# Optimization experiments

Hardware: AMD Instinct MI355X
Metric: run time of the kernel (lower is better)

The kernel has to match this reference:

```python
import jax, jax.numpy as jnp
import numpy as np

N_NODES = 100000


def _gcn_layer(x, W, b, row, col, ew, n):
    # PyG GCNConv: x' = D^{-1/2} (A + I) D^{-1/2} (x W) + b
    xw = x @ W  # [N, out]
    deg = jax.ops.segment_sum(ew, col, num_segments=n)  # weighted in-degree incl. self loops
    dinv = jnp.where(deg > 0, jax.lax.rsqrt(deg), 0.0)
    norm = dinv[row] * ew * dinv[col]  # [E]
    msg = xw[row] * norm[:, None]  # [E, out] gather + scale
    out = jax.ops.segment_sum(msg, col, num_segments=n) + b
    return out


def setup_inputs() -> dict:
    key = jax.random.key(0)
    k = jax.random.split(key, 6)
    E = 1600000
    h = 64
    x = jax.random.normal(k[0], (N_NODES, 4), dtype=jnp.float32)
    edge_index = jax.random.randint(k[1], (2, E), 0, N_NODES, dtype=jnp.int64)
    edge_weight = jax.random.uniform(k[2], (E,), dtype=jnp.float32)
    W1 = jax.random.normal(k[3], (4, h), dtype=jnp.float32) * (1.0 / np.sqrt(4))
    b1 = jnp.zeros((h,), dtype=jnp.float32)
    W2 = jax.random.normal(k[4], (h, h), dtype=jnp.float32) * (1.0 / np.sqrt(h))
    b2 = jnp.zeros((h,), dtype=jnp.float32)
    return {"x": x, "edge_index": edge_index, "edge_weight": edge_weight,
            "W1": W1, "b1": b1, "W2": W2, "b2": b2}


def reference(x, edge_index, edge_weight, W1, b1, W2, b2):
    n = x.shape[0]
    # add self loops with weight 1 (GCNConv default add_self_loops=True)
    loop = jnp.arange(n, dtype=edge_index.dtype)
    row = jnp.concatenate([edge_index[0], loop])
    col = jnp.concatenate([edge_index[1], loop])
    ew = jnp.concatenate([edge_weight, jnp.ones((n,), dtype=edge_weight.dtype)])
    h = jax.nn.relu(_gcn_layer(x, W1, b1, row, col, ew, n))
    out = jax.nn.relu(_gcn_layer(h, W2, b2, row, col, ew, n))
    return out
```

## Files before the change

kernel.cpp:

```cpp
#include <hip/hip_runtime.h>

#define H 64
#define BKT_SHIFT 7
#define BKT_NODES 128
#define NB 782
#define CAP 2432
#define SC_K 16
#define SC_T 256
#define SC_TILE (SC_K * SC_T)

typedef __attribute__((ext_vector_type(8))) short short8v;
typedef __attribute__((ext_vector_type(4))) float float4v;

__device__ __forceinline__ float bf2f(unsigned short u) {
    return __uint_as_float(((unsigned)u) << 16);
}
__device__ __forceinline__ unsigned short f2bf(float f) {
    unsigned u = __float_as_uint(f);
    unsigned r = ((u >> 16) & 1u) + 0x7FFFu;
    return (unsigned short)((u + r) >> 16);
}
__device__ __forceinline__ float bflo(unsigned d) { return __uint_as_float(d << 16); }
__device__ __forceinline__ float bfhi(unsigned d) { return __uint_as_float(d & 0xFFFF0000u); }


__global__ void k_prep(const float* __restrict__ W2, unsigned* __restrict__ cursor,
                       unsigned short* __restrict__ W2Tb) {
    int g = blockIdx.x * 256 + threadIdx.x;
    if (g < NB) cursor[g] = (unsigned)g * CAP;
    if (g < H * H) {
        int c = g >> 6, k = g & 63;
        W2Tb[g] = f2bf(W2[k * H + c]);
    }
}


__global__ __launch_bounds__(SC_T) void k_bscatter(
        const int* __restrict__ row, const int* __restrict__ col,
        const float* __restrict__ ew, unsigned* __restrict__ cursor,
        uint2* __restrict__ sorted, int E) {
    __shared__ unsigned hist[NB];
    __shared__ unsigned gbase[NB];
    int t = threadIdx.x;
    for (int b = t; b < NB; b += SC_T) hist[b] = 0;
    __syncthreads();
    int tile = blockIdx.x * SC_TILE;
    unsigned st[SC_K];
#pragma unroll
    for (int k = 0; k < SC_K; ++k) {
        int e = tile + k * SC_T + t;
        unsigned enc = 0xFFFFFFFFu;
        if (e < E) {
            unsigned c = (unsigned)col[e];
            unsigned b = c >> BKT_SHIFT;
            unsigned nl = c & (BKT_NODES - 1);
            unsigned r = atomicAdd(&hist[b], 1u);
            enc = (b << 20) | (nl << 13) | r;
        }
        st[k] = enc;
    }
    __syncthreads();
    for (int b = t; b < NB; b += SC_T) {
        unsigned h = hist[b];
        if (h) gbase[b] = atomicAdd(&cursor[b], h);
    }
    __syncthreads();
#pragma unroll
    for (int k = 0; k < SC_K; ++k) {
        int e = tile + k * SC_T + t;
        if (e >= E) continue;
        unsigned enc = st[k];
        unsigned b = enc >> 20, nl = (enc >> 13) & 127u, r = enc & 8191u;
        unsigned pk = ((unsigned)row[e] << 7) | nl;
        sorted[gbase[b] + r] = make_uint2(pk, __float_as_uint(ew[e]));
    }
}


__global__ __launch_bounds__(256) void k_bsort(const uint2* __restrict__ sorted,
                                               const unsigned* __restrict__ cursor,
                                               const float* __restrict__ x,
                                               uint2* __restrict__ sorted2,
                                               unsigned* __restrict__ startA,
                                               unsigned* __restrict__ cntA,
                                               float* __restrict__ dinv,
                                               unsigned short* __restrict__ xqb, int n) {
    __shared__ unsigned hist[BKT_NODES];
    __shared__ unsigned base_[BKT_NODES];
    __shared__ float deg[BKT_NODES];
    __shared__ unsigned wsum;
    int b = blockIdx.x, t = threadIdx.x;
    if (t < BKT_NODES) { hist[t] = 0; deg[t] = 1.0f; }
    __syncthreads();
    unsigned s = (unsigned)b * CAP, e = cursor[b];
    uint2 st[10];
#pragma unroll
    for (int k = 0; k < 10; ++k) {
        unsigned j = s + (unsigned)t + ((unsigned)k << 8);
        if (j < e) {
            uint2 u = sorted[j];
            st[k] = u;
            unsigned nl = u.x & 127u;
            atomicAdd(&hist[nl], 1u);
            atomicAdd(&deg[nl], __uint_as_float(u.y));
        }
    }
    __syncthreads();
    if (t < BKT_NODES) {
        unsigned v = hist[t];
        unsigned sc = v;
#pragma unroll
        for (int d = 1; d < 64; d <<= 1) {
            unsigned u = __shfl_up(sc, d);
            if ((t & 63) >= d) sc += u;
        }
        if (t == 63) wsum = sc;
        base_[t] = sc - v;
        int node = b * BKT_NODES + t;
        if (node < n) {
            cntA[node] = v;
            float di = rsqrtf(deg[t]);
            dinv[node] = di;
            float4 xv = ((const float4*)x)[node];
            ushort4 o;
            o.x = f2bf(xv.x * di); o.y = f2bf(xv.y * di);
            o.z = f2bf(xv.z * di); o.w = f2bf(xv.w * di);
            ((ushort4*)xqb)[node] = o;
        }
        hist[t] = 0;
    }
    __syncthreads();
    if (t >= 64 && t < BKT_NODES) base_[t] += wsum;
    __syncthreads();
    if (t < BKT_NODES) {
        int node = b * BKT_NODES + t;
        if (node < n) startA[node] = s + base_[t];
    }
    __syncthreads();
#pragma unroll
    for (int k = 0; k < 10; ++k) {
        unsigned j = s + (unsigned)t + ((unsigned)k << 8);
        if (j < e) {
            uint2 u = st[k];
            unsigned nl = u.x & 127u;
            unsigned pos = atomicAdd(&hist[nl], 1u);
            sorted2[s + base_[nl] + pos] = make_uint2(u.x & 0xFFFFFF80u, u.y);
        }
    }
}


__global__ __launch_bounds__(256) void k_agg1(const uint2* __restrict__ sorted2,
                                              const unsigned* __restrict__ startA,
                                              const unsigned* __restrict__ cntA,
                                              const float* __restrict__ dinv,
                                              const unsigned short* __restrict__ xqb,
                                              const float* __restrict__ W1,
                                              const float* __restrict__ b1,
                                              unsigned short* __restrict__ hb, int n) {
    __shared__ float w1s[4 * H];
    __shared__ float b1s[H];
    int t = threadIdx.x;
    if (t < 4 * H) w1s[t] = W1[t];
    if (t < H) b1s[t] = b1[t];
    __syncthreads();
    int wv = (int)(__builtin_amdgcn_readfirstlane(threadIdx.x) >> 6);
    int wid = blockIdx.x * 4 + wv;
    if (wid >= n) return;
    int lane = t & 63;
    int eg = lane >> 1, f2 = lane & 1;
    unsigned s = startA[wid];
    unsigned cnt = cntA[wid];
    float aLo = 0.0f, aHi = 0.0f;
    const char* xq = (const char*)xqb + (f2 << 2);
    for (unsigned b = 0; b < cnt; b += 32) {
        unsigned i = b + (unsigned)eg;
        bool v = i < cnt;
        uint2 p = sorted2[s + (v ? i : 0u)];
        float w = v ? __uint_as_float(p.y) : 0.0f;
        unsigned d = *(const unsigned*)(xq + (p.x >> 4));
        aLo = fmaf(bflo(d), w, aLo);
        aHi = fmaf(bfhi(d), w, aHi);
    }
    aLo += __shfl_xor(aLo, 2);  aHi += __shfl_xor(aHi, 2);
    aLo += __shfl_xor(aLo, 4);  aHi += __shfl_xor(aHi, 4);
    aLo += __shfl_xor(aLo, 8);  aHi += __shfl_xor(aHi, 8);
    aLo += __shfl_xor(aLo, 16); aHi += __shfl_xor(aHi, 16);
    aLo += __shfl_xor(aLo, 32); aHi += __shfl_xor(aHi, 32);
    float a0 = __shfl(aLo, 0), a1 = __shfl(aHi, 0);
    float a2 = __shfl(aLo, 1), a3 = __shfl(aHi, 1);
    uint2 sq = *(const uint2*)(xqb + ((size_t)wid << 2));
    a0 += bflo(sq.x); a1 += bfhi(sq.x);
    a2 += bflo(sq.y); a3 += bfhi(sq.y);
    float hv = a0 * w1s[lane] + a1 * w1s[H + lane] + a2 * w1s[2 * H + lane]
             + a3 * w1s[3 * H + lane];
    hv = dinv[wid] * hv + b1s[lane];
    hb[((size_t)wid << 6) + lane] = f2bf(fmaxf(hv, 0.0f));
}


__global__ __launch_bounds__(256) void k_l2mfma(const unsigned short* __restrict__ hb,
                                                const unsigned short* __restrict__ W2Tb,
                                                const float* __restrict__ dinv,
                                                unsigned short* __restrict__ xs2b, int n) {
    __shared__ unsigned short ht[128 * H];
    __shared__ unsigned short wt[H * H];
    int tid = threadIdx.x;
    int base = blockIdx.x * 128;
    for (int idx = tid; idx < 1024; idx += 256) {
        int r = idx >> 3, c = idx & 7;
        uint4 v = *(const uint4*)(hb + (((size_t)(base + r)) << 6) + (c << 3));
        *(uint4*)(ht + (r << 6) + ((c ^ (r & 7)) << 3)) = v;
    }
    for (int idx = tid; idx < 512; idx += 256) {
        int r = idx >> 3, c = idx & 7;
        uint4 v = *(const uint4*)(W2Tb + (r << 6) + (c << 3));
        *(uint4*)(wt + (r << 6) + ((c ^ (r & 7)) << 3)) = v;
    }
    __syncthreads();
    int lane = tid & 63;
    int wv = tid >> 6;
    int R = wv * 32;
    int lr = lane & 15, lq = lane >> 4;
    short8v a[2][2], b[4][2];
#pragma unroll
    for (int m = 0; m < 2; ++m)
#pragma unroll
        for (int kk = 0; kk < 2; ++kk) {
            int row = R + m * 16 + lr;
            int cl = kk * 4 + lq;
            a[m][kk] = *(const short8v*)(ht + (row << 6) + ((cl ^ (row & 7)) << 3));
        }
#pragma unroll
    for (int nt = 0; nt < 4; ++nt)
#pragma unroll
        for (int kk = 0; kk < 2; ++kk) {
            int row = nt * 16 + lr;
            int cl = kk * 4 + lq;
            b[nt][kk] = *(const short8v*)(wt + (row << 6) + ((cl ^ (row & 7)) << 3));
        }
    float4v acc[2][4] = {};
#pragma unroll
    for (int m = 0; m < 2; ++m)
#pragma unroll
        for (int nt = 0; nt < 4; ++nt)
#pragma unroll
            for (int kk = 0; kk < 2; ++kk)
                acc[m][nt] = __builtin_amdgcn_mfma_f32_16x16x32_bf16(a[m][kk], b[nt][kk],
                                                                     acc[m][nt], 0, 0, 0);
#pragma unroll
    for (int m = 0; m < 2; ++m)
#pragma unroll
        for (int i = 0; i < 4; ++i) {
            int node = base + R + m * 16 + lq * 4 + i;
            if (node < n) {
                float di = dinv[node];
#pragma unroll
                for (int nt = 0; nt < 4; ++nt)
                    xs2b[((size_t)node << 6) + nt * 16 + lr] = f2bf(acc[m][nt][i] * di);
            }
        }
}


__global__ __launch_bounds__(256) void k_agg2(const uint2* __restrict__ sorted2,
                                              const unsigned* __restrict__ startA,
                                              const unsigned* __restrict__ cntA,
                                              const float* __restrict__ dinv,
                                              const unsigned short* __restrict__ xsb,
                                              const float* __restrict__ bias,
                                              float* __restrict__ outf, int n) {
    int wv = (int)(__builtin_amdgcn_readfirstlane(threadIdx.x) >> 6);
    int wid = blockIdx.x * 4 + wv;
    if (wid >= n) return;
    int lane = threadIdx.x & 63;
    int eg = lane >> 3;
    int c8 = lane & 7;
    unsigned s = startA[wid];
    unsigned cnt = cntA[wid];
    float di = dinv[wid];
    const char* xb = (const char*)xsb + (c8 << 4);
    float a0=0.f,a1=0.f,a2=0.f,a3=0.f,a4=0.f,a5=0.f,a6=0.f,a7=0.f;
    for (unsigned b = 0; b < cnt; b += 16) {
        unsigned iA = b + (unsigned)eg;
        bool vA = iA < cnt;
        uint2 pA = sorted2[s + (vA ? iA : 0u)];
        float wA = vA ? __uint_as_float(pA.y) : 0.0f;
        uint4 dA = *(const uint4*)(xb + pA.x);
        unsigned iB = iA + 8u;
        bool vB = iB < cnt;
        uint2 pB = sorted2[s + (vB ? iB : 0u)];
        float wB = vB ? __uint_as_float(pB.y) : 0.0f;
        uint4 dB = *(const uint4*)(xb + pB.x);
        a0 = fmaf(bflo(dA.x), wA, a0); a1 = fmaf(bfhi(dA.x), wA, a1);
        a2 = fmaf(bflo(dA.y), wA, a2); a3 = fmaf(bfhi(dA.y), wA, a3);
        a4 = fmaf(bflo(dA.z), wA, a4); a5 = fmaf(bfhi(dA.z), wA, a5);
        a6 = fmaf(bflo(dA.w), wA, a6); a7 = fmaf(bfhi(dA.w), wA, a7);
        a0 = fmaf(bflo(dB.x), wB, a0); a1 = fmaf(bfhi(dB.x), wB, a1);
        a2 = fmaf(bflo(dB.y), wB, a2); a3 = fmaf(bfhi(dB.y), wB, a3);
        a4 = fmaf(bflo(dB.z), wB, a4); a5 = fmaf(bfhi(dB.z), wB, a5);
        a6 = fmaf(bflo(dB.w), wB, a6); a7 = fmaf(bfhi(dB.w), wB, a7);
    }
    a0 += __shfl_xor(a0, 8); a0 += __shfl_xor(a0, 16); a0 += __shfl_xor(a0, 32);
    a1 += __shfl_xor(a1, 8); a1 += __shfl_xor(a1, 16); a1 += __shfl_xor(a1, 32);
    a2 += __shfl_xor(a2, 8); a2 += __shfl_xor(a2, 16); a2 += __shfl_xor(a2, 32);
    a3 += __shfl_xor(a3, 8); a3 += __shfl_xor(a3, 16); a3 += __shfl_xor(a3, 32);
    a4 += __shfl_xor(a4, 8); a4 += __shfl_xor(a4, 16); a4 += __shfl_xor(a4, 32);
    a5 += __shfl_xor(a5, 8); a5 += __shfl_xor(a5, 16); a5 += __shfl_xor(a5, 32);
    a6 += __shfl_xor(a6, 8); a6 += __shfl_xor(a6, 16); a6 += __shfl_xor(a6, 32);
    a7 += __shfl_xor(a7, 8); a7 += __shfl_xor(a7, 16); a7 += __shfl_xor(a7, 32);
    uint4 sv = *(const uint4*)((const char*)xsb + (((size_t)(unsigned)wid) << 7) + (c8 << 4));
    a0 += bflo(sv.x); a1 += bfhi(sv.x);
    a2 += bflo(sv.y); a3 += bfhi(sv.y);
    a4 += bflo(sv.z); a5 += bfhi(sv.z);
    a6 += bflo(sv.w); a7 += bfhi(sv.w);
    const float* bp = bias + (c8 << 3);
    float r0 = fmaxf(di * a0 + bp[0], 0.0f);
    float r1 = fmaxf(di * a1 + bp[1], 0.0f);
    float r2 = fmaxf(di * a2 + bp[2], 0.0f);
    float r3 = fmaxf(di * a3 + bp[3], 0.0f);
    float r4 = fmaxf(di * a4 + bp[4], 0.0f);
    float r5 = fmaxf(di * a5 + bp[5], 0.0f);
    float r6 = fmaxf(di * a6 + bp[6], 0.0f);
    float r7 = fmaxf(di * a7 + bp[7], 0.0f);
    if (eg == 0) {
        float4 o = {r0, r1, r2, r3};
        *(float4*)(outf + (((size_t)wid) << 6) + (c8 << 3)) = o;
    } else if (eg == 1) {
        float4 o = {r4, r5, r6, r7};
        *(float4*)(outf + (((size_t)wid) << 6) + (c8 << 3) + 4) = o;
    }
}


extern "C" void kernel_launch(void* const* d_in, const int* in_sizes, int n_in,
                              void* d_out, int out_size, void* d_ws, size_t ws_size,
                              hipStream_t stream) {
    const float* x  = (const float*)d_in[0];
    const int*   ei = (const int*)d_in[1];
    const float* ew = (const float*)d_in[2];
    const float* W1 = (const float*)d_in[3];
    const float* b1 = (const float*)d_in[4];
    const float* W2 = (const float*)d_in[5];
    const float* b2 = (const float*)d_in[6];
    float* out = (float*)d_out;

    const int n = in_sizes[0] / 4;
    const int E = in_sizes[2];
    const int* row = ei;
    const int* col = ei + E;

    char* p = (char*)d_ws;
    unsigned* cursor = (unsigned*)p;            p += 1024 * 4;
    unsigned short* W2Tb = (unsigned short*)p;  p += (size_t)H * H * 2;
    float* dinv      = (float*)p;               p += (size_t)n * 4;
    unsigned* startA = (unsigned*)p;            p += (size_t)n * 4;
    unsigned* cntA   = (unsigned*)p;            p += (size_t)n * 4;
    unsigned short* xqb = (unsigned short*)p;   p += (size_t)n * 4 * 2;
    unsigned short* hb  = (unsigned short*)p;   p += ((size_t)n + 128) * H * 2;
    unsigned short* xs2b = (unsigned short*)p;  p += (size_t)n * H * 2;
    uint2* sorted    = (uint2*)p;               p += ((size_t)NB * CAP + 64) * 8;
    uint2* sorted2   = (uint2*)p;

    k_prep<<<16, 256, 0, stream>>>(W2, cursor, W2Tb);

    k_bscatter<<<(E + SC_TILE - 1) / SC_TILE, SC_T, 0, stream>>>(row, col, ew, cursor, sorted, E);

    k_bsort<<<NB, 256, 0, stream>>>(sorted, cursor, x, sorted2, startA, cntA, dinv, xqb, n);

    int aggBlocks = (n + 3) / 4;
    k_agg1<<<aggBlocks, 256, 0, stream>>>(sorted2, startA, cntA, dinv, xqb, W1, b1, hb, n);

    k_l2mfma<<<(n + 127) / 128, 256, 0, stream>>>(hb, W2Tb, dinv, xs2b, n);

    k_agg2<<<aggBlocks, 256, 0, stream>>>(sorted2, startA, cntA, dinv, xs2b, b2, out, n);
}
```

Baseline: 149.6 us.

## Aggregate layer-1 per thread, fuse W1 transform into MFMA kernel, narrow agg2 lanes

```diff
diff --git a/kernel.cpp b/kernel.cpp
--- a/kernel.cpp
+++ b/kernel.cpp
@@ -153,69 +153,90 @@
 __global__ __launch_bounds__(256) void k_agg1(const uint2* __restrict__ sorted2,
                                               const unsigned* __restrict__ startA,
                                               const unsigned* __restrict__ cntA,
-                                              const float* __restrict__ dinv,
                                               const unsigned short* __restrict__ xqb,
-                                              const float* __restrict__ W1,
-                                              const float* __restrict__ b1,
-                                              unsigned short* __restrict__ hb, int n) {
+                                              float4* __restrict__ agg4, int n) {
+    int node = blockIdx.x * 256 + threadIdx.x;
+    if (node >= n) return;
+    unsigned s = startA[node];
+    unsigned cnt = cntA[node];
+    const char* xq = (const char*)xqb;
+    uint2 sq = *(const uint2*)(xqb + ((size_t)node << 2));
+    float a0 = bflo(sq.x), a1 = bfhi(sq.x), a2 = bflo(sq.y), a3 = bfhi(sq.y);
+    unsigned j = 0;
+    for (; j + 4 <= cnt; j += 4) {
+        uint2 p0 = sorted2[s + j + 0];
+        uint2 p1 = sorted2[s + j + 1];
+        uint2 p2 = sorted2[s + j + 2];
+        uint2 p3 = sorted2[s + j + 3];
+        uint2 q0 = *(const uint2*)(xq + (p0.x >> 4));
+        uint2 q1 = *(const uint2*)(xq + (p1.x >> 4));
+        uint2 q2 = *(const uint2*)(xq + (p2.x >> 4));
+        uint2 q3 = *(const uint2*)(xq + (p3.x >> 4));
+        float w0 = __uint_as_float(p0.y), w1 = __uint_as_float(p1.y);
+        float w2 = __uint_as_float(p2.y), w3 = __uint_as_float(p3.y);
+        a0 = fmaf(bflo(q0.x), w0, a0); a1 = fmaf(bfhi(q0.x), w0, a1);
+        a2 = fmaf(bflo(q0.y), w0, a2); a3 = fmaf(bfhi(q0.y), w0, a3);
+        a0 = fmaf(bflo(q1.x), w1, a0); a1 = fmaf(bfhi(q1.x), w1, a1);
+        a2 = fmaf(bflo(q1.y), w1, a2); a3 = fmaf(bfhi(q1.y), w1, a3);
+        a0 = fmaf(bflo(q2.x), w2, a0); a1 = fmaf(bfhi(q2.x), w2, a1);
+        a2 = fmaf(bflo(q2.y), w2, a2); a3 = fmaf(bfhi(q2.y), w2, a3);
+        a0 = fmaf(bflo(q3.x), w3, a0); a1 = fmaf(bfhi(q3.x), w3, a1);
+        a2 = fmaf(bflo(q3.y), w3, a2); a3 = fmaf(bfhi(q3.y), w3, a3);
+    }
+    for (; j < cnt; ++j) {
+        uint2 p = sorted2[s + j];
+        uint2 q = *(const uint2*)(xq + (p.x >> 4));
+        float w = __uint_as_float(p.y);
+        a0 = fmaf(bflo(q.x), w, a0); a1 = fmaf(bfhi(q.x), w, a1);
+        a2 = fmaf(bflo(q.y), w, a2); a3 = fmaf(bfhi(q.y), w, a3);
+    }
+    agg4[node] = make_float4(a0, a1, a2, a3);
+}
+
+
+__global__ __launch_bounds__(256) void k_l2front(const float4* __restrict__ agg4,
+                                                 const float* __restrict__ W1,
+                                                 const float* __restrict__ b1,
+                                                 const unsigned short* __restrict__ W2Tb,
+                                                 const float* __restrict__ dinv,
+                                                 unsigned short* __restrict__ xs2b, int n) {
+    __shared__ unsigned short ht[128 * H];
+    __shared__ unsigned short wt[H * H];
     __shared__ float w1s[4 * H];
     __shared__ float b1s[H];
-    int t = threadIdx.x;
-    if (t < 4 * H) w1s[t] = W1[t];
-    if (t < H) b1s[t] = b1[t];
-    __syncthreads();
-    int wv = (int)(__builtin_amdgcn_readfirstlane(threadIdx.x) >> 6);
-    int wid = blockIdx.x * 4 + wv;
-    if (wid >= n) return;
-    int lane = t & 63;
-    int eg = lane >> 1, f2 = lane & 1;
-    unsigned s = startA[wid];
-    unsigned cnt = cntA[wid];
-    float aLo = 0.0f, aHi = 0.0f;
-    const char* xq = (const char*)xqb + (f2 << 2);
-    for (unsigned b = 0; b < cnt; b += 32) {
-        unsigned i = b + (unsigned)eg;
-        bool v = i < cnt;
-        uint2 p = sorted2[s + (v ? i : 0u)];
-        float w = v ? __uint_as_float(p.y) : 0.0f;
-        unsigned d = *(const unsigned*)(xq + (p.x >> 4));
-        aLo = fmaf(bflo(d), w, aLo);
-        aHi = fmaf(bfhi(d), w, aHi);
-    }
-    aLo += __shfl_xor(aLo, 2);  aHi += __shfl_xor(aHi, 2);
-    aLo += __shfl_xor(aLo, 4);  aHi += __shfl_xor(aHi, 4);
-    aLo += __shfl_xor(aLo, 8);  aHi += __shfl_xor(aHi, 8);
-    aLo += __shfl_xor(aLo, 16); aHi += __shfl_xor(aHi, 16);
-    aLo += __shfl_xor(aLo, 32); aHi += __shfl_xor(aHi, 32);
-    float a0 = __shfl(aLo, 0), a1 = __shfl(aHi, 0);
-    float a2 = __shfl(aLo, 1), a3 = __shfl(aHi, 1);
-    uint2 sq = *(const uint2*)(xqb + ((size_t)wid << 2));
-    a0 += bflo(sq.x); a1 += bfhi(sq.x);
-    a2 += bflo(sq.y); a3 += bfhi(sq.y);
-    float hv = a0 * w1s[lane] + a1 * w1s[H + lane] + a2 * w1s[2 * H + lane]
-             + a3 * w1s[3 * H + lane];
-    hv = dinv[wid] * hv + b1s[lane];
-    hb[((size_t)wid << 6) + lane] = f2bf(fmaxf(hv, 0.0f));
-}
-
-
-__global__ __launch_bounds__(256) void k_l2mfma(const unsigned short* __restrict__ hb,
-                                                const unsigned short* __restrict__ W2Tb,
-                                                const float* __restrict__ dinv,
-                                                unsigned short* __restrict__ xs2b, int n) {
-    __shared__ unsigned short ht[128 * H];
-    __shared__ unsigned short wt[H * H];
     int tid = threadIdx.x;
     int base = blockIdx.x * 128;
-    for (int idx = tid; idx < 1024; idx += 256) {
-        int r = idx >> 3, c = idx & 7;
-        uint4 v = *(const uint4*)(hb + (((size_t)(base + r)) << 6) + (c << 3));
-        *(uint4*)(ht + (r << 6) + ((c ^ (r & 7)) << 3)) = v;
-    }
+    w1s[tid] = W1[tid];
+    if (tid < H) b1s[tid] = b1[tid];
     for (int idx = tid; idx < 512; idx += 256) {
         int r = idx >> 3, c = idx & 7;
         uint4 v = *(const uint4*)(W2Tb + (r << 6) + (c << 3));
         *(uint4*)(wt + (r << 6) + ((c ^ (r & 7)) << 3)) = v;
+    }
+    __syncthreads();
+    {
+        int r = tid >> 1, ch = tid & 1;
+        int node = base + r;
+        float4 av = (node < n) ? agg4[node] : make_float4(0.f, 0.f, 0.f, 0.f);
+        float di = (node < n) ? dinv[node] : 0.0f;
+#pragma unroll
+        for (int cc = 0; cc < 4; ++cc) {
+            int cl = ch * 4 + cc;
+            uint4 ov;
+            unsigned* op = (unsigned*)&ov;
+#pragma unroll
+            for (int d = 0; d < 4; ++d) {
+                int col = (cl << 3) + (d << 1);
+                float h0 = av.x * w1s[col]     + av.y * w1s[H + col]
+                         + av.z * w1s[2*H+col] + av.w * w1s[3*H + col];
+                float h1 = av.x * w1s[col+1]     + av.y * w1s[H + col+1]
+                         + av.z * w1s[2*H+col+1] + av.w * w1s[3*H + col+1];
+                h0 = fmaxf(di * h0 + b1s[col], 0.0f);
+                h1 = fmaxf(di * h1 + b1s[col + 1], 0.0f);
+                op[d] = ((unsigned)f2bf(h1) << 16) | f2bf(h0);
+            }
+            *(uint4*)(ht + (r << 6) + ((cl ^ (r & 7)) << 3)) = ov;
+        }
     }
     __syncthreads();
     int lane = tid & 63;
@@ -274,61 +295,44 @@
     int wid = blockIdx.x * 4 + wv;
     if (wid >= n) return;
     int lane = threadIdx.x & 63;
-    int eg = lane >> 3;
-    int c8 = lane & 7;
+    int eg = lane >> 4;
+    int c16 = lane & 15;
     unsigned s = startA[wid];
     unsigned cnt = cntA[wid];
     float di = dinv[wid];
-    const char* xb = (const char*)xsb + (c8 << 4);
-    float a0=0.f,a1=0.f,a2=0.f,a3=0.f,a4=0.f,a5=0.f,a6=0.f,a7=0.f;
-    for (unsigned b = 0; b < cnt; b += 16) {
+    const char* xb = (const char*)xsb + (c16 << 3);
+    float a0 = 0.f, a1 = 0.f, a2 = 0.f, a3 = 0.f;
+    for (unsigned b = 0; b < cnt; b += 8) {
         unsigned iA = b + (unsigned)eg;
         bool vA = iA < cnt;
         uint2 pA = sorted2[s + (vA ? iA : 0u)];
         float wA = vA ? __uint_as_float(pA.y) : 0.0f;
-        uint4 dA = *(const uint4*)(xb + pA.x);
-        unsigned iB = iA + 8u;
+        uint2 dA = *(const uint2*)(xb + pA.x);
+        unsigned iB = iA + 4u;
         bool vB = iB < cnt;
         uint2 pB = sorted2[s + (vB ? iB : 0u)];
         float wB = vB ? __uint_as_float(pB.y) : 0.0f;
-        uint4 dB = *(const uint4*)(xb + pB.x);
+        uint2 dB = *(const uint2*)(xb + pB.x);
         a0 = fmaf(bflo(dA.x), wA, a0); a1 = fmaf(bfhi(dA.x), wA, a1);
         a2 = fmaf(bflo(dA.y), wA, a2); a3 = fmaf(bfhi(dA.y), wA, a3);
-        a4 = fmaf(bflo(dA.z), wA, a4); a5 = fmaf(bfhi(dA.z), wA, a5);
-        a6 = fmaf(bflo(dA.w), wA, a6); a7 = fmaf(bfhi(dA.w), wA, a7);
         a0 = fmaf(bflo(dB.x), wB, a0); a1 = fmaf(bfhi(dB.x), wB, a1);
         a2 = fmaf(bflo(dB.y), wB, a2); a3 = fmaf(bfhi(dB.y), wB, a3);
-        a4 = fmaf(bflo(dB.z), wB, a4); a5 = fmaf(bfhi(dB.z), wB, a5);
-        a6 = fmaf(bflo(dB.w), wB, a6); a7 = fmaf(bfhi(dB.w), wB, a7);
-    }
-    a0 += __shfl_xor(a0, 8); a0 += __shfl_xor(a0, 16); a0 += __shfl_xor(a0, 32);
-    a1 += __shfl_xor(a1, 8); a1 += __shfl_xor(a1, 16); a1 += __shfl_xor(a1, 32);
-    a2 += __shfl_xor(a2, 8); a2 += __shfl_xor(a2, 16); a2 += __shfl_xor(a2, 32);
-    a3 += __shfl_xor(a3, 8); a3 += __shfl_xor(a3, 16); a3 += __shfl_xor(a3, 32);
-    a4 += __shfl_xor(a4, 8); a4 += __shfl_xor(a4, 16); a4 += __shfl_xor(a4, 32);
-    a5 += __shfl_xor(a5, 8); a5 += __shfl_xor(a5, 16); a5 += __shfl_xor(a5, 32);
-    a6 += __shfl_xor(a6, 8); a6 += __shfl_xor(a6, 16); a6 += __shfl_xor(a6, 32);
-    a7 += __shfl_xor(a7, 8); a7 += __shfl_xor(a7, 16); a7 += __shfl_xor(a7, 32);
-    uint4 sv = *(const uint4*)((const char*)xsb + (((size_t)(unsigned)wid) << 7) + (c8 << 4));
-    a0 += bflo(sv.x); a1 += bfhi(sv.x);
-    a2 += bflo(sv.y); a3 += bfhi(sv.y);
-    a4 += bflo(sv.z); a5 += bfhi(sv.z);
-    a6 += bflo(sv.w); a7 += bfhi(sv.w);
-    const float* bp = bias + (c8 << 3);
-    float r0 = fmaxf(di * a0 + bp[0], 0.0f);
-    float r1 = fmaxf(di * a1 + bp[1], 0.0f);
-    float r2 = fmaxf(di * a2 + bp[2], 0.0f);
-    float r3 = fmaxf(di * a3 + bp[3], 0.0f);
-    float r4 = fmaxf(di * a4 + bp[4], 0.0f);
-    float r5 = fmaxf(di * a5 + bp[5], 0.0f);
-    float r6 = fmaxf(di * a6 + bp[6], 0.0f);
-    float r7 = fmaxf(di * a7 + bp[7], 0.0f);
+    }
+    a0 += __shfl_xor(a0, 16); a0 += __shfl_xor(a0, 32);
+    a1 += __shfl_xor(a1, 16); a1 += __shfl_xor(a1, 32);
+    a2 += __shfl_xor(a2, 16); a2 += __shfl_xor(a2, 32);
+    a3 += __shfl_xor(a3, 16); a3 += __shfl_xor(a3, 32);
     if (eg == 0) {
-        float4 o = {r0, r1, r2, r3};
-        *(float4*)(outf + (((size_t)wid) << 6) + (c8 << 3)) = o;
-    } else if (eg == 1) {
-        float4 o = {r4, r5, r6, r7};
-        *(float4*)(outf + (((size_t)wid) << 6) + (c8 << 3) + 4) = o;
+        uint2 sv = *(const uint2*)((const char*)xsb + (((size_t)(unsigned)wid) << 7) + (c16 << 3));
+        a0 += bflo(sv.x); a1 += bfhi(sv.x);
+        a2 += bflo(sv.y); a3 += bfhi(sv.y);
+        float4 bp = *(const float4*)(bias + (c16 << 2));
+        float4 o;
+        o.x = fmaxf(di * a0 + bp.x, 0.0f);
+        o.y = fmaxf(di * a1 + bp.y, 0.0f);
+        o.z = fmaxf(di * a2 + bp.z, 0.0f);
+        o.w = fmaxf(di * a3 + bp.w, 0.0f);
+        *(float4*)(outf + (((size_t)wid) << 6) + (c16 << 2)) = o;
     }
 }
 
@@ -357,7 +361,7 @@
     unsigned* startA = (unsigned*)p;            p += (size_t)n * 4;
     unsigned* cntA   = (unsigned*)p;            p += (size_t)n * 4;
     unsigned short* xqb = (unsigned short*)p;   p += (size_t)n * 4 * 2;
-    unsigned short* hb  = (unsigned short*)p;   p += ((size_t)n + 128) * H * 2;
+    float4* agg4     = (float4*)p;              p += ((size_t)n + 128) * 16;
     unsigned short* xs2b = (unsigned short*)p;  p += (size_t)n * H * 2;
     uint2* sorted    = (uint2*)p;               p += ((size_t)NB * CAP + 64) * 8;
     uint2* sorted2   = (uint2*)p;
@@ -368,10 +372,9 @@
 
     k_bsort<<<NB, 256, 0, stream>>>(sorted, cursor, x, sorted2, startA, cntA, dinv, xqb, n);
 
-    int aggBlocks = (n + 3) / 4;
-    k_agg1<<<aggBlocks, 256, 0, stream>>>(sorted2, startA, cntA, dinv, xqb, W1, b1, hb, n);
-
-    k_l2mfma<<<(n + 127) / 128, 256, 0, stream>>>(hb, W2Tb, dinv, xs2b, n);
-
-    k_agg2<<<aggBlocks, 256, 0, stream>>>(sorted2, startA, cntA, dinv, xs2b, b2, out, n);
-}
+    k_agg1<<<(n + 255) / 256, 256, 0, stream>>>(sorted2, startA, cntA, xqb, agg4, n);
+
+    k_l2front<<<(n + 127) / 128, 256, 0, stream>>>(agg4, W1, b1, W2Tb, dinv, xs2b, n);
+
+    k_agg2<<<(n + 3) / 4, 256, 0, stream>>>(sorted2, startA, cntA, dinv, xs2b, b2, out, n);
+}
```

Measured after the change: 138.2 us. 7.6% less time.
